# Kernel optimization log

Hardware: AMD Instinct MI355X
Metric: run time of the kernel (lower is better)

The kernel has to match this reference:

```python
import jax, jax.numpy as jnp
import numpy as np

D_MODEL = 1024
NUM_HEADS = 16
HEAD_DIM = D_MODEL // NUM_HEADS


def setup_inputs() -> dict:
    key = jax.random.key(0)
    ks = jax.random.split(key, 10)
    B, SQ, SKV = 4, 2048, 2048
    s = 1.0 / np.sqrt(D_MODEL)
    return {
        "query": jax.random.normal(ks[0], (B, SQ, D_MODEL), jnp.float32),
        "key_value": jax.random.normal(ks[1], (B, SKV, D_MODEL), jnp.float32),
        "Wq": jax.random.normal(ks[2], (D_MODEL, D_MODEL), jnp.float32) * s,
        "bq": jnp.zeros((D_MODEL,), jnp.float32),
        "Wk": jax.random.normal(ks[3], (D_MODEL, D_MODEL), jnp.float32) * s,
        "bk": jnp.zeros((D_MODEL,), jnp.float32),
        "Wv": jax.random.normal(ks[4], (D_MODEL, D_MODEL), jnp.float32) * s,
        "bv": jnp.zeros((D_MODEL,), jnp.float32),
        "Wo": jax.random.normal(ks[5], (D_MODEL, D_MODEL), jnp.float32) * s,
        "bo": jnp.zeros((D_MODEL,), jnp.float32),
    }


def reference(query, key_value, Wq, bq, Wk, bk, Wv, bv, Wo, bo):
    B, SQ, _ = query.shape
    SKV = key_value.shape[1]
    H, Dh = NUM_HEADS, HEAD_DIM
    # projections (torch Linear: x @ W.T + b); split heads -> (B, H, S, Dh)
    Q = (query @ Wq.T + bq).reshape(B, SQ, H, Dh).transpose(0, 2, 1, 3)
    K = (key_value @ Wk.T + bk).reshape(B, SKV, H, Dh).transpose(0, 2, 1, 3)
    V = (key_value @ Wv.T + bv).reshape(B, SKV, H, Dh).transpose(0, 2, 1, 3)
    scale = jnp.asarray(np.sqrt(Dh), query.dtype)
    scores = jnp.einsum("bhqd,bhkd->bhqk", Q, K) / scale
    weights = jax.nn.softmax(scores, axis=-1)  # dropout is identity in eval
    attn = jnp.einsum("bhqk,bhkd->bhqd", weights, V)
    attn = attn.transpose(0, 2, 1, 3).reshape(B, SQ, H * Dh)
    return attn @ Wo.T + bo
```

## Files before the change

### kernel.cpp

```cpp
#include <hip/hip_runtime.h>

#define NH 16
#define DH 64
#define DM 1024
#define SEQ 2048
#define BATCH 4

typedef short s16x8 __attribute__((ext_vector_type(8)));
typedef float f32x4 __attribute__((ext_vector_type(4)));

__device__ __forceinline__ unsigned short f2bf(float f) {
  union { float f; unsigned int u; } v; v.f = f;
  unsigned int u = v.u;
  unsigned int r = (u + 0x7fffu + ((u >> 16) & 1u)) >> 16;
  return (unsigned short)r;
}

__device__ __forceinline__ unsigned int pkbf(float a, float b) {
#if __has_builtin(__builtin_amdgcn_cvt_pk_bf16_f32)
  typedef short v2s __attribute__((ext_vector_type(2)));
  v2s r = __builtin_amdgcn_cvt_pk_bf16_f32(a, b);
  union { v2s v; unsigned int u; } cv; cv.v = r;
  return cv.u;
#else
  return (unsigned int)f2bf(a) | ((unsigned int)f2bf(b) << 16);
#endif
}

__device__ __forceinline__ float fexp2(float x) {
#if __has_builtin(__builtin_amdgcn_exp2f)
  return __builtin_amdgcn_exp2f(x);
#else
  return exp2f(x);
#endif
}

__device__ __forceinline__ void gload_lds16(const void* g, void* l) {
  __builtin_amdgcn_global_load_lds(
      (const __attribute__((address_space(1))) unsigned int*)g,
      (__attribute__((address_space(3))) unsigned int*)l, 16, 0, 0);
}

__global__ void convert_all(const float* __restrict__ q, const float* __restrict__ kv,
                            const float* __restrict__ w0, const float* __restrict__ w1,
                            const float* __restrict__ w2, const float* __restrict__ w3,
                            unsigned short* __restrict__ oq, unsigned short* __restrict__ okv,
                            unsigned short* __restrict__ ow0, unsigned short* __restrict__ ow1,
                            unsigned short* __restrict__ ow2, unsigned short* __restrict__ ow3) {
  const int NQ4 = (BATCH * SEQ * DM) / 4;
  const int NW4 = (DM * DM) / 4;
  const int total = NQ4 * 2 + NW4 * 4;
  for (int i = blockIdx.x * blockDim.x + threadIdx.x; i < total;
       i += gridDim.x * blockDim.x) {
    const float* s; unsigned short* d; int off;
    if (i < NQ4)            { s = q;  d = oq;  off = i; }
    else if (i < 2 * NQ4)   { s = kv; d = okv; off = i - NQ4; }
    else {
      int j = i - 2 * NQ4; int wsel = j / NW4; off = j - wsel * NW4;
      s = (wsel == 0) ? w0 : (wsel == 1) ? w1 : (wsel == 2) ? w2 : w3;
      d = (wsel == 0) ? ow0 : (wsel == 1) ? ow1 : (wsel == 2) ? ow2 : ow3;
    }
    float4 v = *(const float4*)(s + (size_t)off * 4);
    ushort4 o;
    o.x = f2bf(v.x); o.y = f2bf(v.y); o.z = f2bf(v.z); o.w = f2bf(v.w);
    *(ushort4*)(d + (size_t)off * 4) = o;
  }
}

__device__ __forceinline__ void gemm_tile(const unsigned short* __restrict__ X,
                                          const unsigned short* __restrict__ Wt,
                                          unsigned short* As, unsigned short* Bs,
                                          int m0, int n0, f32x4 (*acc)[4]) {
  const int tid = threadIdx.x;
  const int wv_ = tid >> 6, lane = tid & 63;
  const int quad = lane >> 4, c = lane & 15;
  const int wm = (wv_ >> 1) * 64, wn = (wv_ & 1) * 64;
  const int srow = lane >> 3;
  const int scol = ((lane & 7) ^ srow) * 8;

  for (int kt = 0; kt < DM; kt += 64) {
#pragma unroll
    for (int i = 0; i < 4; ++i) {
      int reg = wv_ * 4 + i;
      gload_lds16(X + (size_t)(m0 + reg * 8 + srow) * DM + kt + scol,
                  (void*)(As + reg * 512));
      gload_lds16(Wt + (size_t)(n0 + reg * 8 + srow) * DM + kt + scol,
                  (void*)(Bs + reg * 512));
    }
    __syncthreads();
#pragma unroll
    for (int k2 = 0; k2 < 2; ++k2) {
      s16x8 a[4], b[4];
      int g = k2 * 4 + quad;
#pragma unroll
      for (int t = 0; t < 4; ++t)
        a[t] = *(const s16x8*)(As + (wm + t * 16 + c) * 64 + ((g ^ (c & 7)) * 8));
#pragma unroll
      for (int t = 0; t < 4; ++t)
        b[t] = *(const s16x8*)(Bs + (wn + t * 16 + c) * 64 + ((g ^ (c & 7)) * 8));
#pragma unroll
      for (int tm = 0; tm < 4; ++tm)
#pragma unroll
        for (int tn = 0; tn < 4; ++tn)
          acc[tm][tn] = __builtin_amdgcn_mfma_f32_16x16x32_bf16(
              a[tm], b[tn], acc[tm][tn], 0, 0, 0);
    }
    __syncthreads();
  }
}

__global__ __launch_bounds__(256)
void gemm_qkv(const unsigned short* __restrict__ Xq,
              const unsigned short* __restrict__ Xkv,
              const unsigned short* __restrict__ W0,
              const unsigned short* __restrict__ W1,
              const unsigned short* __restrict__ W2,
              const float* __restrict__ b0, const float* __restrict__ b1,
              const float* __restrict__ b2,
              unsigned short* __restrict__ OQ, unsigned short* __restrict__ OK_,
              unsigned short* __restrict__ OV) {
  __shared__ alignas(16) unsigned short As[128 * 64];
  __shared__ alignas(16) unsigned short Bs[128 * 64];
  const int m0 = blockIdx.x * 128;
  const int ysel = blockIdx.y >> 3;
  const int n0 = (blockIdx.y & 7) * 128;
  const unsigned short* X = (ysel == 0) ? Xq : Xkv;
  const unsigned short* Wt = (ysel == 0) ? W0 : (ysel == 1) ? W1 : W2;
  const float* bias = (ysel == 0) ? b0 : (ysel == 1) ? b1 : b2;
  unsigned short* Out = (ysel == 0) ? OQ : (ysel == 1) ? OK_ : OV;
  const float scale = (ysel == 0) ? 0.1803368801f : 1.0f;

  f32x4 acc[4][4] = {};
  gemm_tile(X, Wt, As, Bs, m0, n0, acc);

  const int tid = threadIdx.x;
  const int wv_ = tid >> 6, lane = tid & 63;
  const int quad = lane >> 4, c = lane & 15;
  const int wm = (wv_ >> 1) * 64, wn = (wv_ & 1) * 64;
#pragma unroll
  for (int tm = 0; tm < 4; ++tm) {
#pragma unroll
    for (int tn = 0; tn < 4; ++tn) {
      int n = n0 + wn + tn * 16 + c;
      float bv = bias[n];
      int m_base = m0 + wm + tm * 16 + quad * 4;
      if (ysel == 2) {
        int b_ = m_base >> 11, s_ = m_base & 2047, h_ = n >> 6, dh = n & 63;
        size_t idx = (((size_t)(b_ * NH + h_)) * DH + dh) * SEQ + s_;
        ushort4 o4;
        o4.x = f2bf(acc[tm][tn][0] + bv);
        o4.y = f2bf(acc[tm][tn][1] + bv);
        o4.z = f2bf(acc[tm][tn][2] + bv);
        o4.w = f2bf(acc[tm][tn][3] + bv);
        *(ushort4*)(&Out[idx]) = o4;
      } else {
#pragma unroll
        for (int p = 0; p < 4; ++p) {
          int m = m_base + p;
          float val = (acc[tm][tn][p] + bv) * scale;
          int b_ = m >> 11, s_ = m & 2047, h_ = n >> 6, dh = n & 63;
          size_t idx = (((size_t)(b_ * NH + h_)) * SEQ + s_) * DH + dh;
          Out[idx] = f2bf(val);
        }
      }
    }
  }
}

__global__ __launch_bounds__(256)
void gemm_o(const unsigned short* __restrict__ X,
            const unsigned short* __restrict__ Wt,
            const float* __restrict__ bias, float* __restrict__ Out) {
  __shared__ alignas(16) unsigned short As[128 * 64];
  __shared__ alignas(16) unsigned short Bs[128 * 64];
  const int m0 = blockIdx.x * 128;
  const int n0 = blockIdx.y * 128;
  f32x4 acc[4][4] = {};
  gemm_tile(X, Wt, As, Bs, m0, n0, acc);

  const int tid = threadIdx.x;
  const int wv_ = tid >> 6, lane = tid & 63;
  const int quad = lane >> 4, c = lane & 15;
  const int wm = (wv_ >> 1) * 64, wn = (wv_ & 1) * 64;
#pragma unroll
  for (int tm = 0; tm < 4; ++tm) {
#pragma unroll
    for (int tn = 0; tn < 4; ++tn) {
      int n = n0 + wn + tn * 16 + c;
      float bv = bias[n];
#pragma unroll
      for (int p = 0; p < 4; ++p) {
        int m = m0 + wm + tm * 16 + quad * 4 + p;
        Out[(size_t)m * DM + n] = acc[tm][tn][p] + bv;
      }
    }
  }
}

__global__ __launch_bounds__(512, 2)
void attn_kernel(const unsigned short* __restrict__ Qb,
                 const unsigned short* __restrict__ Kb,
                 const unsigned short* __restrict__ VTb,
                 unsigned short* __restrict__ Ob) {
  __shared__ alignas(16) unsigned short SM[32768];

  const int tid = threadIdx.x, wv_ = tid >> 6, lane = tid & 63;
  const int quad = lane >> 4, c = lane & 15;
  const int wg = blockIdx.x;
  const int bh = (wg & 7) + 8 * ((wg >> 3) >> 2);
  const int qb = (wg >> 3) & 3;
  const unsigned short* Qp = Qb + (size_t)bh * SEQ * DH;
  const unsigned short* Kp = Kb + (size_t)bh * SEQ * DH;
  const unsigned short* Vp = VTb + (size_t)bh * DH * SEQ;
  const int wq0 = qb * 512 + wv_ * 64;

  s16x8 aq[4][2];
#pragma unroll
  for (int t = 0; t < 4; ++t)
#pragma unroll
    for (int k2 = 0; k2 < 2; ++k2)
      aq[t][k2] = *(const s16x8*)(Qp + (size_t)(wq0 + t * 16 + c) * DH +
                                  k2 * 32 + quad * 8);

  f32x4 ot[4][4] = {};
  f32x4 lacc[4] = {};
  s16x8 ones;
  {
    union { s16x8 v; unsigned short u[8]; } o_;
#pragma unroll
    for (int j = 0; j < 8; ++j) o_.u[j] = 0x3F80;
    ones = o_.v;
  }

  const int srow = lane >> 3;
  const int ch = ((lane & 7) ^ (srow & 3)) ^ ((wv_ & 1) << 2);

  const int fK = (c & 3) | (((c >> 2) & 1) << 2);
  const int fV = (c & 3) | (((c >> 3) & 1) << 2);

#define STAGE_TILE(ktt, buf)                                                   \
  {                                                                            \
    gload_lds16(Kp + (size_t)((ktt) + wv_ * 8 + srow) * DH + ch * 8,           \
                (void*)(SM + (buf) * 8192 + wv_ * 512));                       \
    gload_lds16(Kp + (size_t)((ktt) + 64 + wv_ * 8 + srow) * DH + ch * 8,      \
                (void*)(SM + (buf) * 8192 + 4096 + wv_ * 512));                \
    gload_lds16(Vp + (size_t)(wv_ * 8 + srow) * SEQ + (ktt) + ch * 8,          \
                (void*)(SM + 16384 + (buf) * 8192 + wv_ * 512));               \
    gload_lds16(Vp + (size_t)(wv_ * 8 + srow) * SEQ + (ktt) + 64 + ch * 8,     \
                (void*)(SM + 16384 + (buf) * 8192 + 4096 + wv_ * 512));        \
  }

  STAGE_TILE(0, 0);

  for (int kt = 0; kt < SEQ; kt += 128) {
    const int cur = (kt >> 7) & 1;
    __syncthreads();
    if (kt + 128 < SEQ) STAGE_TILE(kt + 128, cur ^ 1);

#pragma unroll
    for (int kh = 0; kh < 2; ++kh) {
      const unsigned short* K_ = SM + cur * 8192 + kh * 4096;
      const unsigned short* V_ = SM + 16384 + cur * 8192 + kh * 4096;

      f32x4 s[4][2][2] = {};
#pragma unroll
      for (int k2 = 0; k2 < 2; ++k2) {
        s16x8 ak[2][2];
#pragma unroll
        for (int jp = 0; jp < 2; ++jp)
#pragma unroll
          for (int h = 0; h < 2; ++h) {
            int r = jp * 32 + ((c >> 2) << 3) + h * 4 + (c & 3);
            int g = k2 * 4 + quad;
            ak[jp][h] = *(const s16x8*)(K_ + r * 64 + ((g ^ fK) * 8));
          }
        __builtin_amdgcn_s_setprio(1);
#pragma unroll
        for (int t = 0; t < 4; ++t)
#pragma unroll
          for (int jp = 0; jp < 2; ++jp)
#pragma unroll
            for (int h = 0; h < 2; ++h)
              s[t][jp][h] = __builtin_amdgcn_mfma_f32_16x16x32_bf16(
                  ak[jp][h], aq[t][k2], s[t][jp][h], 0, 0, 0);
        __builtin_amdgcn_s_setprio(0);
      }

      s16x8 bp[4][2];
#pragma unroll
      for (int t = 0; t < 4; ++t)
#pragma unroll
        for (int jp = 0; jp < 2; ++jp) {
          float e00 = fexp2(s[t][jp][0][0]);
          float e01 = fexp2(s[t][jp][0][1]);
          float e02 = fexp2(s[t][jp][0][2]);
          float e03 = fexp2(s[t][jp][0][3]);
          float e10 = fexp2(s[t][jp][1][0]);
          float e11 = fexp2(s[t][jp][1][1]);
          float e12 = fexp2(s[t][jp][1][2]);
          float e13 = fexp2(s[t][jp][1][3]);
          union { s16x8 v; unsigned int u[4]; } pk;
          pk.u[0] = pkbf(e00, e01);
          pk.u[1] = pkbf(e02, e03);
          pk.u[2] = pkbf(e10, e11);
          pk.u[3] = pkbf(e12, e13);
          bp[t][jp] = pk.v;
          lacc[t] = __builtin_amdgcn_mfma_f32_16x16x32_bf16(
              ones, bp[t][jp], lacc[t], 0, 0, 0);
        }

#pragma unroll
      for (int jp = 0; jp < 2; ++jp)
#pragma unroll
        for (int dt = 0; dt < 4; ++dt) {
          int g = jp * 4 + quad;
          int r = dt * 16 + c;
          s16x8 av = *(const s16x8*)(V_ + r * 64 + ((g ^ fV) * 8));
          __builtin_amdgcn_s_setprio(1);
#pragma unroll
          for (int t = 0; t < 4; ++t)
            ot[dt][t] = __builtin_amdgcn_mfma_f32_16x16x32_bf16(
                av, bp[t][jp], ot[dt][t], 0, 0, 0);
          __builtin_amdgcn_s_setprio(0);
        }
    }
  }

  __syncthreads();

  const int b_ = bh >> 4, h_ = bh & 15;
  const int ql = lane >> 1, hf = lane & 1;
  unsigned short* Lq = SM + wv_ * (32 * 72);
#pragma unroll
  for (int half = 0; half < 2; ++half) {
    if (half) asm volatile("s_waitcnt lgkmcnt(0)" ::: "memory");
#pragma unroll
    for (int t2 = 0; t2 < 2; ++t2) {
      int t = half * 2 + t2;
      float inv = 1.0f / lacc[t][0];
#pragma unroll
      for (int dt = 0; dt < 4; ++dt) {
        unsigned int w01 = pkbf(ot[dt][t][0] * inv, ot[dt][t][1] * inv);
        unsigned int w23 = pkbf(ot[dt][t][2] * inv, ot[dt][t][3] * inv);
        unsigned short* p = Lq + (t2 * 16 + c) * 72 + dt * 16 + quad * 4;
        *(unsigned int*)(p) = w01;
        *(unsigned int*)(p + 2) = w23;
      }
    }
    const unsigned short* Lr = Lq + ql * 72 + hf * 32;
    unsigned short* Og = Ob + ((size_t)(b_ * SEQ + wq0 + half * 32 + ql)) * DM +
                         h_ * 64 + hf * 32;
#pragma unroll
    for (int j = 0; j < 4; ++j) {
      s16x8 v = *(const s16x8*)(Lr + j * 8);
      *(s16x8*)(Og + j * 8) = v;
    }
  }
#undef STAGE_TILE
}

extern "C" void kernel_launch(void* const* d_in, const int* in_sizes, int n_in,
                              void* d_out, int out_size, void* d_ws, size_t ws_size,
                              hipStream_t stream) {
  const float* q  = (const float*)d_in[0];
  const float* kv = (const float*)d_in[1];
  const float* Wq = (const float*)d_in[2];
  const float* bq = (const float*)d_in[3];
  const float* Wk = (const float*)d_in[4];
  const float* bk = (const float*)d_in[5];
  const float* Wv = (const float*)d_in[6];
  const float* bv = (const float*)d_in[7];
  const float* Wo = (const float*)d_in[8];
  const float* bo = (const float*)d_in[9];

  char* ws = (char*)d_ws;
  const size_t MB = 1024 * 1024;
  unsigned short* q_bf  = (unsigned short*)(ws);
  unsigned short* kv_bf = (unsigned short*)(ws + 16 * MB);
  unsigned short* wq_bf = (unsigned short*)(ws + 32 * MB);
  unsigned short* wk_bf = (unsigned short*)(ws + 34 * MB);
  unsigned short* wv_bf = (unsigned short*)(ws + 36 * MB);
  unsigned short* wo_bf = (unsigned short*)(ws + 38 * MB);
  unsigned short* Qb    = (unsigned short*)(ws + 40 * MB);
  unsigned short* Kb    = (unsigned short*)(ws + 56 * MB);
  unsigned short* VTb   = (unsigned short*)(ws + 72 * MB);
  unsigned short* attn  = (unsigned short*)(ws + 88 * MB);

  convert_all<<<2048, 256, 0, stream>>>(q, kv, Wq, Wk, Wv, Wo,
                                        q_bf, kv_bf, wq_bf, wk_bf, wv_bf, wo_bf);
  gemm_qkv<<<dim3(64, 24), 256, 0, stream>>>(q_bf, kv_bf, wq_bf, wk_bf, wv_bf,
                                             bq, bk, bv, Qb, Kb, VTb);
  attn_kernel<<<dim3(256), 512, 0, stream>>>(Qb, Kb, VTb, attn);
  gemm_o<<<dim3(64, 8), 256, 0, stream>>>(attn, wo_bf, bo, (float*)d_out);
}
```

Measured before the change: 304.9 us.

## Load K and V fragments directly from global memory instead of LDS staging

The attention kernel drops its double-buffered LDS staging of K and V tiles and the per-tile barriers. Each wave now reads its K and V MFMA fragments straight from global memory, relying on L1/L2 caching, and the shared buffer shrinks to what the output epilogue needs. This removes LDS traffic and synchronisation, but the eight waves in a block no longer share loads. That means redundant global/L2 reads and exposed load latency with no explicit prefetch.

```diff
diff --git a/kernel.cpp b/kernel.cpp
--- a/kernel.cpp
+++ b/kernel.cpp
@@ -202,7 +202,7 @@
                  const unsigned short* __restrict__ Kb,
                  const unsigned short* __restrict__ VTb,
                  unsigned short* __restrict__ Ob) {
-  __shared__ alignas(16) unsigned short SM[32768];
+  __shared__ alignas(16) unsigned short SM[18432];
 
   const int tid = threadIdx.x, wv_ = tid >> 6, lane = tid & 63;
   const int quad = lane >> 4, c = lane & 15;
@@ -232,101 +232,69 @@
     ones = o_.v;
   }
 
-  const int srow = lane >> 3;
-  const int ch = ((lane & 7) ^ (srow & 3)) ^ ((wv_ & 1) << 2);
-
-  const int fK = (c & 3) | (((c >> 2) & 1) << 2);
-  const int fV = (c & 3) | (((c >> 3) & 1) << 2);
-
-#define STAGE_TILE(ktt, buf)                                                   \
-  {                                                                            \
-    gload_lds16(Kp + (size_t)((ktt) + wv_ * 8 + srow) * DH + ch * 8,           \
-                (void*)(SM + (buf) * 8192 + wv_ * 512));                       \
-    gload_lds16(Kp + (size_t)((ktt) + 64 + wv_ * 8 + srow) * DH + ch * 8,      \
-                (void*)(SM + (buf) * 8192 + 4096 + wv_ * 512));                \
-    gload_lds16(Vp + (size_t)(wv_ * 8 + srow) * SEQ + (ktt) + ch * 8,          \
-                (void*)(SM + 16384 + (buf) * 8192 + wv_ * 512));               \
-    gload_lds16(Vp + (size_t)(wv_ * 8 + srow) * SEQ + (ktt) + 64 + ch * 8,     \
-                (void*)(SM + 16384 + (buf) * 8192 + 4096 + wv_ * 512));        \
-  }
-
-  STAGE_TILE(0, 0);
-
-  for (int kt = 0; kt < SEQ; kt += 128) {
-    const int cur = (kt >> 7) & 1;
-    __syncthreads();
-    if (kt + 128 < SEQ) STAGE_TILE(kt + 128, cur ^ 1);
-
-#pragma unroll
-    for (int kh = 0; kh < 2; ++kh) {
-      const unsigned short* K_ = SM + cur * 8192 + kh * 4096;
-      const unsigned short* V_ = SM + 16384 + cur * 8192 + kh * 4096;
-
-      f32x4 s[4][2][2] = {};
-#pragma unroll
-      for (int k2 = 0; k2 < 2; ++k2) {
-        s16x8 ak[2][2];
+  const int r0 = ((c >> 2) << 3) + (c & 3);
+  const int kbase = r0 * 64 + quad * 8;
+  const int vbase = c * SEQ + quad * 8;
+
+  for (int kt = 0; kt < SEQ; kt += 64) {
+    f32x4 s[4][2][2] = {};
+#pragma unroll
+    for (int k2 = 0; k2 < 2; ++k2) {
+      s16x8 ak[2][2];
+#pragma unroll
+      for (int jp = 0; jp < 2; ++jp)
+#pragma unroll
+        for (int h = 0; h < 2; ++h)
+          ak[jp][h] = *(const s16x8*)(Kp + kt * 64 + kbase + jp * 2048 +
+                                      h * 256 + k2 * 32);
+      __builtin_amdgcn_s_setprio(1);
+#pragma unroll
+      for (int t = 0; t < 4; ++t)
 #pragma unroll
         for (int jp = 0; jp < 2; ++jp)
 #pragma unroll
-          for (int h = 0; h < 2; ++h) {
-            int r = jp * 32 + ((c >> 2) << 3) + h * 4 + (c & 3);
-            int g = k2 * 4 + quad;
-            ak[jp][h] = *(const s16x8*)(K_ + r * 64 + ((g ^ fK) * 8));
-          }
+          for (int h = 0; h < 2; ++h)
+            s[t][jp][h] = __builtin_amdgcn_mfma_f32_16x16x32_bf16(
+                ak[jp][h], aq[t][k2], s[t][jp][h], 0, 0, 0);
+      __builtin_amdgcn_s_setprio(0);
+    }
+
+    s16x8 bp[4][2];
+#pragma unroll
+    for (int t = 0; t < 4; ++t)
+#pragma unroll
+      for (int jp = 0; jp < 2; ++jp) {
+        float e00 = fexp2(s[t][jp][0][0]);
+        float e01 = fexp2(s[t][jp][0][1]);
+        float e02 = fexp2(s[t][jp][0][2]);
+        float e03 = fexp2(s[t][jp][0][3]);
+        float e10 = fexp2(s[t][jp][1][0]);
+        float e11 = fexp2(s[t][jp][1][1]);
+        float e12 = fexp2(s[t][jp][1][2]);
+        float e13 = fexp2(s[t][jp][1][3]);
+        union { s16x8 v; unsigned int u[4]; } pk;
+        pk.u[0] = pkbf(e00, e01);
+        pk.u[1] = pkbf(e02, e03);
+        pk.u[2] = pkbf(e10, e11);
+        pk.u[3] = pkbf(e12, e13);
+        bp[t][jp] = pk.v;
+        lacc[t] = __builtin_amdgcn_mfma_f32_16x16x32_bf16(
+            ones, bp[t][jp], lacc[t], 0, 0, 0);
+      }
+
+#pragma unroll
+    for (int jp = 0; jp < 2; ++jp)
+#pragma unroll
+      for (int dt = 0; dt < 4; ++dt) {
+        s16x8 av = *(const s16x8*)(Vp + vbase + dt * 16 * SEQ + kt + jp * 32);
         __builtin_amdgcn_s_setprio(1);
 #pragma unroll
         for (int t = 0; t < 4; ++t)
-#pragma unroll
-          for (int jp = 0; jp < 2; ++jp)
-#pragma unroll
-            for (int h = 0; h < 2; ++h)
-              s[t][jp][h] = __builtin_amdgcn_mfma_f32_16x16x32_bf16(
-                  ak[jp][h], aq[t][k2], s[t][jp][h], 0, 0, 0);
+          ot[dt][t] = __builtin_amdgcn_mfma_f32_16x16x32_bf16(
+              av, bp[t][jp], ot[dt][t], 0, 0, 0);
         __builtin_amdgcn_s_setprio(0);
       }
-
-      s16x8 bp[4][2];
-#pragma unroll
-      for (int t = 0; t < 4; ++t)
-#pragma unroll
-        for (int jp = 0; jp < 2; ++jp) {
-          float e00 = fexp2(s[t][jp][0][0]);
-          float e01 = fexp2(s[t][jp][0][1]);
-          float e02 = fexp2(s[t][jp][0][2]);
-          float e03 = fexp2(s[t][jp][0][3]);
-          float e10 = fexp2(s[t][jp][1][0]);
-          float e11 = fexp2(s[t][jp][1][1]);
-          float e12 = fexp2(s[t][jp][1][2]);
-          float e13 = fexp2(s[t][jp][1][3]);
-          union { s16x8 v; unsigned int u[4]; } pk;
-          pk.u[0] = pkbf(e00, e01);
-          pk.u[1] = pkbf(e02, e03);
-          pk.u[2] = pkbf(e10, e11);
-          pk.u[3] = pkbf(e12, e13);
-          bp[t][jp] = pk.v;
-          lacc[t] = __builtin_amdgcn_mfma_f32_16x16x32_bf16(
-              ones, bp[t][jp], lacc[t], 0, 0, 0);
-        }
-
-#pragma unroll
-      for (int jp = 0; jp < 2; ++jp)
-#pragma unroll
-        for (int dt = 0; dt < 4; ++dt) {
-          int g = jp * 4 + quad;
-          int r = dt * 16 + c;
-          s16x8 av = *(const s16x8*)(V_ + r * 64 + ((g ^ fV) * 8));
-          __builtin_amdgcn_s_setprio(1);
-#pragma unroll
-          for (int t = 0; t < 4; ++t)
-            ot[dt][t] = __builtin_amdgcn_mfma_f32_16x16x32_bf16(
-                av, bp[t][jp], ot[dt][t], 0, 0, 0);
-          __builtin_amdgcn_s_setprio(0);
-        }
-    }
-  }
-
-  __syncthreads();
+  }
 
   const int b_ = bh >> 4, h_ = bh & 15;
   const int ql = lane >> 1, hf = lane & 1;
@@ -356,7 +324,6 @@
       *(s16x8*)(Og + j * 8) = v;
     }
   }
-#undef STAGE_TILE
 }
 
 extern "C" void kernel_launch(void* const* d_in, const int* in_sizes, int n_in,
```

After: 362.3 us. 1.19x slower.
